# Kernel optimization log

Hardware: AMD Instinct MI355X
Metric: run time of the kernel (lower is better)

## Reference

```python
import jax, jax.numpy as jnp
import numpy as np

N = 100000      # nodes
E = 1600000     # edges
F_IN = 128
HID = 128
N_CLS = 40
KEEP = 0.5      # 1 - dropout p
NORM_BIAS = 0.0


def setup_inputs() -> dict:
    key = jax.random.key(0)
    ks = jax.random.split(key, 12)
    features = jax.random.normal(ks[0], (N, F_IN), jnp.float32)
    src = jax.random.randint(ks[1], (E,), 0, N, jnp.int32)
    dst = jax.random.randint(ks[2], (E,), 0, N, jnp.int32)
    mask1 = jax.random.randint(ks[3], (N, HID), 0, 2) == 1
    mask2 = jax.random.randint(ks[4], (N, HID), 0, 2) == 1
    # Glorot-ish weights, zero bias (as in DGL GraphConv defaults)
    w0 = jax.random.normal(ks[5], (F_IN, HID), jnp.float32) / np.sqrt(F_IN)
    b0 = jnp.zeros((HID,), jnp.float32)
    w1 = jax.random.normal(ks[6], (HID, HID), jnp.float32) / np.sqrt(HID)
    b1 = jnp.zeros((HID,), jnp.float32)
    w2 = jax.random.normal(ks[7], (HID, N_CLS), jnp.float32) / np.sqrt(HID)
    b2 = jnp.zeros((N_CLS,), jnp.float32)
    return {"features": features, "src": src, "dst": dst,
            "mask1": mask1, "mask2": mask2,
            "w0": w0, "b0": b0, "w1": w1, "b1": b1, "w2": w2, "b2": b2}


def _graph_conv(h, w, b, src, dst, norm, act):
    # GraphConv: linear -> SpMM (sum over in-edges) -> right norm -> bias -> act
    h = h @ w                                       # [N, d_out]
    agg = jax.ops.segment_sum(h[src], dst, num_segments=N)  # copy_u/sum SpMM
    h = agg * norm[:, None] + b
    return jax.nn.relu(h) if act else h


def reference(features, src, dst, mask1, mask2, w0, b0, w1, b1, w2, b2):
    # right normalization: 1 / (in_degree + norm_bias), degree clamped to >= 1
    deg = jax.ops.segment_sum(jnp.ones((E,), jnp.float32), dst, num_segments=N)
    norm = 1.0 / (jnp.maximum(deg, 1.0) + NORM_BIAS)

    h = _graph_conv(features, w0, b0, src, dst, norm, act=True)
    h = jnp.where(mask1, h / KEEP, 0.0)   # dropout (inverted, deterministic mask)
    h = _graph_conv(h, w1, b1, src, dst, norm, act=True)
    h = jnp.where(mask2, h / KEEP, 0.0)
    h = _graph_conv(h, w2, b2, src, dst, norm, act=False)
    return h
```

## Files before the change

kernel.cpp:

```cpp
#include <hip/hip_runtime.h>


#define PAD 64

typedef short short8 __attribute__((ext_vector_type(8)));
typedef float f32x4 __attribute__((ext_vector_type(4)));

__device__ __forceinline__ unsigned short f2bf(float f) {
    unsigned u = __float_as_uint(f);
    return (unsigned short)((u + 0x7fffu + ((u >> 16) & 1u)) >> 16);
}

__global__ __launch_bounds__(256) void k_init(int* __restrict__ cnt, int n,
                                              const unsigned* __restrict__ m,
                                              int* __restrict__ flag,
                                              const float* __restrict__ W1,
                                              const float* __restrict__ W2,
                                              unsigned short* __restrict__ W1T,
                                              unsigned short* __restrict__ W2T) {
    int base = blockIdx.x * 1024 + threadIdx.x * 4;
#pragma unroll
    for (int j = 0; j < 4; ++j) {
        int i = base + j;
        if (i < n) cnt[i] = 0;
    }
    if (blockIdx.x < 4) {
        unsigned v = m[blockIdx.x * 256 + threadIdx.x];
        if (v > 1u) atomicOr(flag, 1);
    }
    int g = blockIdx.x * 256 + threadIdx.x;
    if (g < 128 * 128) {
        int k = g >> 7, c = g & 127;
        W1T[c * 128 + k] = f2bf(W1[g]);
    }
    if (g < 48 * 128) {
        int c = g >> 7, k = g & 127;
        W2T[g] = (c < 40) ? f2bf(W2[k * 40 + c]) : (unsigned short)0;
    }
}

__global__ __launch_bounds__(256) void k_g0scat(
        const float* __restrict__ X, const float* __restrict__ Wg,
        unsigned short* __restrict__ Y, int nrows, int gb,
        const int* __restrict__ src, const int* __restrict__ dst,
        int* __restrict__ cnt, int* __restrict__ slots, int E) {
    __shared__ float Xs[64][32];
    __shared__ float Ws[32][128];
    int bid = blockIdx.x;
    int t = threadIdx.x;

    bool isg = (bid < gb * 5) && ((bid % 5) == 4);
    if (!isg) {
        int sblk = (bid < gb * 5) ? (bid / 5) * 4 + (bid % 5)
                                  : gb * 4 + (bid - gb * 5);
        int e = sblk * 256 + t;
        if (e < E) {
            int d = dst[e];
            int p = atomicAdd(&cnt[d], 1);
            if (p < PAD) slots[(size_t)d * PAD + p] = src[e];
        }
        return;
    }

    int bm = (bid / 5) * 64;
    int tx = t & 15, ty = t >> 4;
    int sw = ((ty >> 1) & 3) << 2;
    float acc[4][8];
#pragma unroll
    for (int i = 0; i < 4; ++i)
#pragma unroll
        for (int j = 0; j < 8; ++j) acc[i][j] = 0.0f;

    for (int kc = 0; kc < 128; kc += 32) {
        for (int idx = t; idx < 64 * 8; idx += 256) {
            int row = idx >> 3, k4 = idx & 7;
            int grow = bm + row;
            if (grow >= nrows) grow = nrows - 1;
            float4 v = *(const float4*)(X + (size_t)grow * 128 + kc + k4 * 4);
            int kk2 = (k4 * 4) ^ (((row >> 3) & 3) << 2);
            *(float4*)&Xs[row][kk2] = v;
        }
        for (int idx = t; idx < 32 * 32; idx += 256) {
            int k = idx >> 5, c4 = idx & 31;
            *(float4*)&Ws[k][c4 * 4] =
                *(const float4*)(Wg + (size_t)(kc + k) * 128 + c4 * 4);
        }
        __syncthreads();

        for (int k = 0; k < 32; k += 4) {
            float4 a4[4];
#pragma unroll
            for (int i = 0; i < 4; ++i)
                a4[i] = *(const float4*)&Xs[ty * 4 + i][k ^ sw];
#pragma unroll
            for (int kk = 0; kk < 4; ++kk) {
                float b[8];
                *(float4*)&b[0] = *(const float4*)&Ws[k + kk][tx * 4];
                *(float4*)&b[4] = *(const float4*)&Ws[k + kk][64 + tx * 4];
#pragma unroll
                for (int i = 0; i < 4; ++i) {
                    float a = ((const float*)&a4[i])[kk];
#pragma unroll
                    for (int j = 0; j < 8; ++j) acc[i][j] += a * b[j];
                }
            }
        }
        __syncthreads();
    }

#pragma unroll
    for (int i = 0; i < 4; ++i) {
        int r = bm + ty * 4 + i;
        if (r < nrows) {
            ushort4 u0, u1;
            u0.x = f2bf(acc[i][0]); u0.y = f2bf(acc[i][1]);
            u0.z = f2bf(acc[i][2]); u0.w = f2bf(acc[i][3]);
            u1.x = f2bf(acc[i][4]); u1.y = f2bf(acc[i][5]);
            u1.z = f2bf(acc[i][6]); u1.w = f2bf(acc[i][7]);
            *(ushort4*)(Y + (size_t)r * 128 + tx * 4) = u0;
            *(ushort4*)(Y + (size_t)r * 128 + 64 + tx * 4) = u1;
        }
    }
}

template<int BN>
__global__ __launch_bounds__(256) void k_mfma(
        const unsigned short* __restrict__ Xg,
        const unsigned short* __restrict__ WT,
        unsigned short* __restrict__ Yout, int N, int ldo) {
    constexpr int CT = BN / 16;
    __shared__ unsigned short Xs[128][128];
    __shared__ unsigned short Ws[BN][128];
    int t = threadIdx.x;
    int bm = blockIdx.x * 128;

    for (int idx = t; idx < 128 * 16; idx += 256) {
        int row = idx >> 4, c = idx & 15;
        int grow = bm + row;
        if (grow >= N) grow = N - 1;
        uint4 v = *(const uint4*)(Xg + (size_t)grow * 128 + c * 8);
        *(uint4*)&Xs[row][(c ^ (row & 15)) * 8] = v;
    }
    for (int idx = t; idx < BN * 16; idx += 256) {
        int row = idx >> 4, c = idx & 15;
        uint4 v = *(const uint4*)(WT + (size_t)row * 128 + c * 8);
        *(uint4*)&Ws[row][(c ^ (row & 15)) * 8] = v;
    }
    __syncthreads();

    int l = t & 63, w = t >> 6;
    int lr = l & 15, lg = l >> 4;
    f32x4 acc[2][CT];
#pragma unroll
    for (int rt = 0; rt < 2; ++rt)
#pragma unroll
        for (int ct = 0; ct < CT; ++ct) acc[rt][ct] = (f32x4)0.0f;

#pragma unroll
    for (int ks = 0; ks < 4; ++ks) {
        int cc = (ks * 4 + lg) ^ lr;
        short8 a0 = *(const short8*)&Xs[w * 32 + lr][cc * 8];
        short8 a1 = *(const short8*)&Xs[w * 32 + 16 + lr][cc * 8];
#pragma unroll
        for (int ct = 0; ct < CT; ++ct) {
            short8 b = *(const short8*)&Ws[ct * 16 + lr][cc * 8];
            acc[0][ct] = __builtin_amdgcn_mfma_f32_16x16x32_bf16(a0, b, acc[0][ct], 0, 0, 0);
            acc[1][ct] = __builtin_amdgcn_mfma_f32_16x16x32_bf16(a1, b, acc[1][ct], 0, 0, 0);
        }
    }

#pragma unroll
    for (int rt = 0; rt < 2; ++rt)
#pragma unroll
        for (int ct = 0; ct < CT; ++ct)
#pragma unroll
            for (int i = 0; i < 4; ++i) {
                int r = bm + w * 32 + rt * 16 + lg * 4 + i;
                int col = ct * 16 + lr;
                if (r < N && (BN == 128 || col < 40))
                    Yout[(size_t)r * ldo + col] = f2bf(acc[rt][ct][i]);
            }
}

__global__ __launch_bounds__(256) void k_spmmw(const unsigned* __restrict__ Y,
                       const int* __restrict__ cnt, const int* __restrict__ slots,
                       const float* __restrict__ bias,
                       const void* __restrict__ mask, const int* __restrict__ mflag,
                       unsigned* __restrict__ H, int N) {
    int wid = threadIdx.x >> 6;
    int lane = threadIdx.x & 63;
    int i = blockIdx.x * 4 + wid;
    if (i >= N) return;
    int c = lane * 2;
    int d0 = cnt[i];
    int d = d0 > PAD ? PAD : d0;
    const int* row = slots + (size_t)i * PAD;
    float2 acc = {0.0f, 0.0f};
    int e = 0;
    for (; e + 3 < d; e += 4) {
        unsigned u0 = Y[(size_t)row[e] * 64 + lane];
        unsigned u1 = Y[(size_t)row[e + 1] * 64 + lane];
        unsigned u2 = Y[(size_t)row[e + 2] * 64 + lane];
        unsigned u3 = Y[(size_t)row[e + 3] * 64 + lane];
        acc.x += __uint_as_float(u0 << 16) + __uint_as_float(u1 << 16)
               + __uint_as_float(u2 << 16) + __uint_as_float(u3 << 16);
        acc.y += __uint_as_float(u0 & 0xffff0000u) + __uint_as_float(u1 & 0xffff0000u)
               + __uint_as_float(u2 & 0xffff0000u) + __uint_as_float(u3 & 0xffff0000u);
    }
    for (; e < d; ++e) {
        unsigned u = Y[(size_t)row[e] * 64 + lane];
        acc.x += __uint_as_float(u << 16);
        acc.y += __uint_as_float(u & 0xffff0000u);
    }
    float nrm = 1.0f / fmaxf((float)d0, 1.0f);
    float2 b = *(const float2*)&bias[c];
    float vx = fmaxf(acc.x * nrm + b.x, 0.0f);
    float vy = fmaxf(acc.y * nrm + b.y, 0.0f);
    size_t j = (size_t)i * 128 + c;
    bool k0, k1;
    if (*mflag != 0) {
        const unsigned char* m = (const unsigned char*)mask;
        k0 = m[j] != 0; k1 = m[j + 1] != 0;
    } else {
        const int* m = (const int*)mask;
        k0 = m[j] != 0; k1 = m[j + 1] != 0;
    }
    vx = k0 ? vx * 2.0f : 0.0f;
    vy = k1 ? vy * 2.0f : 0.0f;
    H[(size_t)i * 64 + lane] =
        (unsigned)f2bf(vx) | ((unsigned)f2bf(vy) << 16);
}

__global__ __launch_bounds__(256) void k_spmm40w(const unsigned* __restrict__ Y,
                        const int* __restrict__ cnt, const int* __restrict__ slots,
                        const float* __restrict__ bias,
                        float* __restrict__ H, int N, int width) {
    int wid = threadIdx.x >> 6;
    int lane = threadIdx.x & 63;
    int i = blockIdx.x * 4 + wid;
    if (i >= N) return;
    int c = lane * 2;
    if (c >= width) return;
    int d0 = cnt[i];
    int d = d0 > PAD ? PAD : d0;
    const int* row = slots + (size_t)i * PAD;
    float2 acc = {0.0f, 0.0f};
    int e = 0;
    for (; e + 3 < d; e += 4) {
        unsigned u0 = Y[(size_t)row[e] * 20 + lane];
        unsigned u1 = Y[(size_t)row[e + 1] * 20 + lane];
        unsigned u2 = Y[(size_t)row[e + 2] * 20 + lane];
        unsigned u3 = Y[(size_t)row[e + 3] * 20 + lane];
        acc.x += __uint_as_float(u0 << 16) + __uint_as_float(u1 << 16)
               + __uint_as_float(u2 << 16) + __uint_as_float(u3 << 16);
        acc.y += __uint_as_float(u0 & 0xffff0000u) + __uint_as_float(u1 & 0xffff0000u)
               + __uint_as_float(u2 & 0xffff0000u) + __uint_as_float(u3 & 0xffff0000u);
    }
    for (; e < d; ++e) {
        unsigned u = Y[(size_t)row[e] * 20 + lane];
        acc.x += __uint_as_float(u << 16);
        acc.y += __uint_as_float(u & 0xffff0000u);
    }
    float nrm = 1.0f / fmaxf((float)d0, 1.0f);
    float vx = acc.x * nrm + bias[c];
    float vy = acc.y * nrm + bias[c + 1];
    *(float2*)(H + (size_t)i * width + c) = make_float2(vx, vy);
}

extern "C" void kernel_launch(void* const* d_in, const int* in_sizes, int n_in,
                              void* d_out, int out_size, void* d_ws, size_t ws_size,
                              hipStream_t stream) {
    const float* feat = (const float*)d_in[0];
    const int* src = (const int*)d_in[1];
    const int* dst = (const int*)d_in[2];
    const void* mask1 = d_in[3];
    const void* mask2 = d_in[4];
    const float* w0 = (const float*)d_in[5];
    const float* b0 = (const float*)d_in[6];
    const float* w1 = (const float*)d_in[7];
    const float* b1 = (const float*)d_in[8];
    const float* w2 = (const float*)d_in[9];
    const float* b2 = (const float*)d_in[10];
    int N = in_sizes[0] / 128;
    int E = in_sizes[1];
    int ncls = in_sizes[10];

    float* out = (float*)d_out;
    unsigned short* A = (unsigned short*)d_ws;
    unsigned short* B = A + (size_t)N * 128;
    int* slots = (int*)(B + (size_t)N * 128);
    int* cnt = slots + (size_t)N * PAD;
    int* mflag = cnt + N;
    unsigned short* W1T = (unsigned short*)(cnt + N + 4);
    unsigned short* W2T = W1T + 128 * 128;

    int nb = (N + 1023) / 1024;

    hipMemsetAsync(mflag, 0, 4, stream);
    k_init<<<nb, 256, 0, stream>>>(cnt, N, (const unsigned*)mask1, mflag,
                                   w1, w2, W1T, W2T);

    int eb = (E + 255) / 256;
    int gb64 = (N + 63) / 64;
    int scap = gb64 * 4;
    int extra = (eb > scap) ? (eb - scap) : 0;
    k_g0scat<<<gb64 * 5 + extra, 256, 0, stream>>>(feat, w0, A, N, gb64,
                                                   src, dst, cnt, slots, E);

    int gb128 = (N + 127) / 128;
    int sb = (N + 3) / 4;
    k_spmmw<<<sb, 256, 0, stream>>>((const unsigned*)A, cnt, slots, b0,
                                    mask1, mflag, (unsigned*)B, N);
    k_mfma<128><<<gb128, 256, 0, stream>>>(B, W1T, A, N, 128);
    k_spmmw<<<sb, 256, 0, stream>>>((const unsigned*)A, cnt, slots, b1,
                                    mask2, mflag, (unsigned*)B, N);
    k_mfma<48><<<gb128, 256, 0, stream>>>(B, W2T, A, N, ncls);
    k_spmm40w<<<sb, 256, 0, stream>>>((const unsigned*)A, cnt, slots, b2,
                                      out, N, ncls);
}
```

Measured before the change: 357.1 us.

## Shard edge bucketing by destination range per XCD with work-stealing windows

The edge-scatter blocks no longer handle a fixed edge range. Each block reads its XCD id and pulls 2048-edge windows from per-shard atomic counters, processing only edges whose destination falls in that shard's node range. The goal is to keep each cnt/slots region's atomics local to one XCD's L2 and avoid cross-XCD contention. In exchange, every shard re-reads the entire dst array (8x the dst reads), and the shard width is hardcoded to 12500 nodes, which assumes N=100000.

```diff
diff --git a/kernel.cpp b/kernel.cpp
--- a/kernel.cpp
+++ b/kernel.cpp
@@ -2,6 +2,9 @@
 
 
 #define PAD 64
+#define NSHARD 8
+#define SHARD_DIV 12500
+#define WIN 2048
 
 typedef short short8 __attribute__((ext_vector_type(8)));
 typedef float f32x4 __attribute__((ext_vector_type(4)));
@@ -14,6 +17,7 @@
 __global__ __launch_bounds__(256) void k_init(int* __restrict__ cnt, int n,
                                               const unsigned* __restrict__ m,
                                               int* __restrict__ flag,
+                                              int* __restrict__ cur,
                                               const float* __restrict__ W1,
                                               const float* __restrict__ W2,
                                               unsigned short* __restrict__ W1T,
@@ -24,6 +28,7 @@
         int i = base + j;
         if (i < n) cnt[i] = 0;
     }
+    if (blockIdx.x == 0 && threadIdx.x < NSHARD) cur[threadIdx.x] = 0;
     if (blockIdx.x < 4) {
         unsigned v = m[blockIdx.x * 256 + threadIdx.x];
         if (v > 1u) atomicOr(flag, 1);
@@ -41,25 +46,49 @@
 
 __global__ __launch_bounds__(256) void k_g0scat(
         const float* __restrict__ X, const float* __restrict__ Wg,
-        unsigned short* __restrict__ Y, int nrows, int gb,
+        unsigned short* __restrict__ Y, int nrows, int gb, int nwin,
         const int* __restrict__ src, const int* __restrict__ dst,
-        int* __restrict__ cnt, int* __restrict__ slots, int E) {
+        int* __restrict__ cnt, int* __restrict__ slots, int* __restrict__ cur,
+        int E) {
     __shared__ float Xs[64][32];
     __shared__ float Ws[32][128];
+    __shared__ int sw_, ss_;
     int bid = blockIdx.x;
     int t = threadIdx.x;
 
     bool isg = (bid < gb * 5) && ((bid % 5) == 4);
     if (!isg) {
-        int sblk = (bid < gb * 5) ? (bid / 5) * 4 + (bid % 5)
-                                  : gb * 4 + (bid - gb * 5);
-        int e = sblk * 256 + t;
-        if (e < E) {
-            int d = dst[e];
-            int p = atomicAdd(&cnt[d], 1);
-            if (p < PAD) slots[(size_t)d * PAD + p] = src[e];
-        }
-        return;
+        int xcd;
+        asm volatile("s_getreg_b32 %0, hwreg(HW_REG_XCC_ID, 0, 4)" : "=s"(xcd));
+        xcd &= 7;
+        for (;;) {
+            if (t == 0) {
+                int w = -1, s = xcd;
+                for (int trial = 0; trial < NSHARD; ++trial) {
+                    int ss = (xcd + trial) & 7;
+                    int ww = atomicAdd(&cur[ss], 1);
+                    if (ww < nwin) { w = ww; s = ss; break; }
+                }
+                sw_ = w; ss_ = s;
+            }
+            __syncthreads();
+            int w = sw_, s = ss_;
+            __syncthreads();
+            if (w < 0) return;
+            int lo = s * SHARD_DIV, hi = lo + SHARD_DIV;
+            int base = w * WIN + t;
+#pragma unroll
+            for (int j = 0; j < 8; ++j) {
+                int e = base + j * 256;
+                if (e < E) {
+                    int d = dst[e];
+                    if (d >= lo && d < hi) {
+                        int p = atomicAdd(&cnt[d], 1);
+                        if (p < PAD) slots[(size_t)d * PAD + p] = src[e];
+                    }
+                }
+            }
+        }
     }
 
     int bm = (bid / 5) * 64;
@@ -291,21 +320,20 @@
     int* slots = (int*)(B + (size_t)N * 128);
     int* cnt = slots + (size_t)N * PAD;
     int* mflag = cnt + N;
-    unsigned short* W1T = (unsigned short*)(cnt + N + 4);
+    int* cur = mflag + 1;
+    unsigned short* W1T = (unsigned short*)(cnt + N + 16);
     unsigned short* W2T = W1T + 128 * 128;
 
     int nb = (N + 1023) / 1024;
 
     hipMemsetAsync(mflag, 0, 4, stream);
-    k_init<<<nb, 256, 0, stream>>>(cnt, N, (const unsigned*)mask1, mflag,
+    k_init<<<nb, 256, 0, stream>>>(cnt, N, (const unsigned*)mask1, mflag, cur,
                                    w1, w2, W1T, W2T);
 
-    int eb = (E + 255) / 256;
+    int nwin = (E + WIN - 1) / WIN;
     int gb64 = (N + 63) / 64;
-    int scap = gb64 * 4;
-    int extra = (eb > scap) ? (eb - scap) : 0;
-    k_g0scat<<<gb64 * 5 + extra, 256, 0, stream>>>(feat, w0, A, N, gb64,
-                                                   src, dst, cnt, slots, E);
+    k_g0scat<<<gb64 * 5, 256, 0, stream>>>(feat, w0, A, N, gb64, nwin,
+                                           src, dst, cnt, slots, cur, E);
 
     int gb128 = (N + 127) / 128;
     int sb = (N + 3) / 4;
```

Measured after the change: 944.1 us. 2.64x slower.
